# Kernel optimization log

Measured on AMD Instinct MI355X. Metric: run time of the kernel, lower is better.

The kernel has to match this reference:

```python
import jax, jax.numpy as jnp
import numpy as np

N_ENTITIES = 100000
N_USERS = 50000
CHANNEL = 64
N_RELATIONS = 16
N_FACTORS = 4
N_EDGES = 1600000
N_INTER = 1000000


def setup_inputs() -> dict:
    key = jax.random.key(0)
    ks = jax.random.split(key, 11)
    return {
        "entity_emb": jax.random.normal(ks[0], (N_ENTITIES, CHANNEL), dtype=jnp.float32),
        "user_emb": jax.random.normal(ks[1], (N_USERS, CHANNEL), dtype=jnp.float32),
        "latent_emb": jax.random.normal(ks[2], (N_FACTORS, CHANNEL), dtype=jnp.float32),
        "weight": jax.random.normal(ks[3], (N_RELATIONS, CHANNEL), dtype=jnp.float32),
        "disen_weight_att": jax.random.normal(ks[4], (N_FACTORS, N_RELATIONS), dtype=jnp.float32),
        "interact_vals": jax.random.uniform(ks[5], (N_INTER,), dtype=jnp.float32),
        "head": jax.random.randint(ks[6], (N_EDGES,), 0, N_ENTITIES),
        "tail": jax.random.randint(ks[7], (N_EDGES,), 0, N_ENTITIES),
        # edge_type is 1-indexed in the original (weight[edge_type - 1])
        "edge_type": jax.random.randint(ks[8], (N_EDGES,), 1, N_RELATIONS + 1),
        "interact_rows": jax.random.randint(ks[9], (N_INTER,), 0, N_USERS),
        "interact_cols": jax.random.randint(ks[10], (N_INTER,), 0, N_ENTITIES),
    }


def reference(entity_emb, user_emb, latent_emb, weight, disen_weight_att,
              interact_vals, head, tail, edge_type, interact_rows, interact_cols):
    # ---- KG aggregate (GATED_ATT branch, vectorized; chunk loop is math-identical) ----
    rel = weight[edge_type - 1]                                  # [E, C]
    att = jax.nn.sigmoid(jnp.sum(entity_emb[head] * rel, axis=1))[:, None]  # [E, 1]
    neigh = att * (entity_emb[tail] * rel)                       # [E, C]
    seg_sum = jax.ops.segment_sum(neigh, head, num_segments=N_ENTITIES)     # [N_e, C]
    cnt = jax.ops.segment_sum(jnp.ones_like(att[:, 0]), head, num_segments=N_ENTITIES)
    entity_agg = seg_sum / jnp.maximum(cnt, 1.0)[:, None]        # scatter_mean (0 if empty)

    # ---- user aggregate ----
    score = jax.nn.softmax(user_emb @ latent_emb.T, axis=1)[:, :, None]      # [U, F, 1]
    user_agg = jax.ops.segment_sum(interact_vals[:, None] * entity_emb[interact_cols],
                                   interact_rows, num_segments=N_USERS)      # sparse mm
    disen = jax.nn.softmax(disen_weight_att, axis=-1) @ weight               # [F, C]
    gate = jnp.sum(disen[None, :, :] * score, axis=1)                        # [U, C]
    user_agg = user_agg * gate + user_agg
    return entity_agg, user_agg
```

## Files before the change

### kernel.cpp

```cpp
#include <hip/hip_runtime.h>

#define N_ENTITIES 100000
#define N_USERS 50000
#define CHANNEL 64
#define N_RELATIONS 16
#define N_FACTORS 4
#define N_EDGES 1600000
#define N_INTER 1000000
#define TMASK ((1 << 17) - 1)

#define BSH 6
#define BSZ 64
#define NBE 1563
#define NBU 782
#define CAP_E 1536
#define CAP_U 1792
#define TILE_E 4096
#define TILE_U 4096
#define NTBE 391
#define NTBU 245
#define NCONV 6250
#define NHIST 256

typedef unsigned short u16;

__device__ __forceinline__ float wave_reduce_sum(float p) {
    #pragma unroll
    for (int off = 32; off > 0; off >>= 1) p += __shfl_xor(p, off);
    return p;
}

__device__ __forceinline__ int block_scan_incl(int v, int* wsum) {
    int lane = threadIdx.x & 63, wid = threadIdx.x >> 6;
    int x = v;
    #pragma unroll
    for (int off = 1; off < 64; off <<= 1) {
        int y = __shfl_up(x, off);
        if (lane >= off) x += y;
    }
    __syncthreads();
    if (lane == 63) wsum[wid] = x;
    __syncthreads();
    if (wid == 0) {
        int s = (lane < 16) ? wsum[lane] : 0;
        #pragma unroll
        for (int off = 1; off < 16; off <<= 1) {
            int y = __shfl_up(s, off);
            if (lane >= off) s += y;
        }
        if (lane < 16) wsum[lane] = s;
    }
    __syncthreads();
    return x + (wid ? wsum[wid - 1] : 0);
}

__device__ __forceinline__ u16 f32_to_bf16_rne(float x) {
    unsigned u = __float_as_uint(x);
    return (u16)((u + 0x7FFFu + ((u >> 16) & 1u)) >> 16);
}

template <bool BF16>
__device__ __forceinline__ float ldrow(const float* __restrict__ e32,
                                       const u16* __restrict__ e16,
                                       int row, int lane) {
    if (BF16) return __uint_as_float(((unsigned)e16[(size_t)row * CHANNEL + lane]) << 16);
    return e32[(size_t)row * CHANNEL + lane];
}

__device__ __forceinline__ void disen_body(const float* __restrict__ dwa,
                                           const float* __restrict__ weight,
                                           float* __restrict__ disen) {
    int f = threadIdx.x >> 6;
    int c = threadIdx.x & 63;
    float m = -INFINITY;
    #pragma unroll
    for (int r = 0; r < N_RELATIONS; ++r) m = fmaxf(m, dwa[f * N_RELATIONS + r]);
    float denom = 0.f, acc = 0.f;
    #pragma unroll
    for (int r = 0; r < N_RELATIONS; ++r) {
        float e = expf(dwa[f * N_RELATIONS + r] - m);
        denom += e;
        acc += e * weight[r * CHANNEL + c];
    }
    disen[f * CHANNEL + c] = acc / denom;
}

__global__ void disen_kernel(const float* __restrict__ dwa,
                             const float* __restrict__ weight,
                             float* __restrict__ disen) {
    disen_body(dwa, weight, disen);
}

__global__ __launch_bounds__(256) void prep_kernel(
    const float* __restrict__ src, u16* __restrict__ dst,
    const float* __restrict__ dwa, const float* __restrict__ weight,
    float* __restrict__ disen,
    const int* __restrict__ head, const int* __restrict__ irows,
    int* __restrict__ wp_e, int* __restrict__ wp_u) {
    __shared__ int lh[NBE + NBU];
    int bid = blockIdx.x;
    int tid = threadIdx.x;
    if (bid < NCONV) {
        int i = bid * 256 + tid;
        float4 v = ((const float4*)src)[i];
        ushort4 o;
        o.x = f32_to_bf16_rne(v.x);
        o.y = f32_to_bf16_rne(v.y);
        o.z = f32_to_bf16_rne(v.z);
        o.w = f32_to_bf16_rne(v.w);
        ((ushort4*)dst)[i] = o;
        return;
    }
    if (bid == NCONV) { disen_body(dwa, weight, disen); return; }
    for (int i = tid; i < NBE + NBU; i += 256) lh[i] = 0;
    __syncthreads();
    const int NTOT = N_EDGES + N_INTER;
    int hb = bid - NCONV - 1;
    for (int i = hb * 256 + tid; i < NTOT; i += NHIST * 256) {
        if (i < N_EDGES) atomicAdd(&lh[head[i] >> BSH], 1);
        else             atomicAdd(&lh[NBE + (irows[i - N_EDGES] >> BSH)], 1);
    }
    __syncthreads();
    for (int i = tid; i < NBE + NBU; i += 256) {
        int c = lh[i];
        if (c) {
            if (i < NBE) atomicAdd(&wp_e[i], c);
            else         atomicAdd(&wp_u[i - NBE], c);
        }
    }
}

__global__ __launch_bounds__(1024) void hist_kernel(
    const int* __restrict__ head, const int* __restrict__ irows,
    int* __restrict__ wp_e, int* __restrict__ wp_u) {
    __shared__ int lh[NBE + NBU];
    int tid = threadIdx.x;
    for (int i = tid; i < NBE + NBU; i += 1024) lh[i] = 0;
    __syncthreads();
    const int NTOT = N_EDGES + N_INTER;
    for (int i = blockIdx.x * 1024 + tid; i < NTOT; i += gridDim.x * 1024) {
        if (i < N_EDGES) atomicAdd(&lh[head[i] >> BSH], 1);
        else             atomicAdd(&lh[NBE + (irows[i - N_EDGES] >> BSH)], 1);
    }
    __syncthreads();
    for (int i = tid; i < NBE + NBU; i += 1024) {
        int c = lh[i];
        if (c) {
            if (i < NBE) atomicAdd(&wp_e[i], c);
            else         atomicAdd(&wp_u[i - NBE], c);
        }
    }
}

__global__ __launch_bounds__(1024) void scan_kernel(
    int* __restrict__ wp_e, int* __restrict__ coff_e,
    int* __restrict__ wp_u, int* __restrict__ coff_u) {
    __shared__ int wsum[16];
    int tid = threadIdx.x;
    int c0 = wp_e[tid];
    int incl0 = block_scan_incl(c0, wsum);
    int tot0 = wsum[15];
    int i1 = 1024 + tid;
    int c1 = (i1 < NBE) ? wp_e[i1] : 0;
    int incl1 = block_scan_incl(c1, wsum) + tot0;
    int cu = (tid < NBU) ? wp_u[tid] : 0;
    int inclu = block_scan_incl(cu, wsum);
    { int ex = incl0 - c0; coff_e[tid] = ex; wp_e[tid] = ex; }
    if (i1 < NBE) { int ex = incl1 - c1; coff_e[i1] = ex; wp_e[i1] = ex; }
    if (tid == 0) coff_e[NBE] = N_EDGES;
    if (tid < NBU) { int ex = inclu - cu; coff_u[tid] = ex; wp_u[tid] = ex; }
    if (tid == 0) coff_u[NBU] = N_INTER;
}

__global__ __launch_bounds__(1024) void scatter_kernel(
    const int* __restrict__ head, const int* __restrict__ tail,
    const int* __restrict__ etype,
    const int* __restrict__ irows, const int* __restrict__ icols,
    const float* __restrict__ vals,
    int* __restrict__ wp_e, int* __restrict__ pay_e,
    int* __restrict__ wp_u, int* __restrict__ payA_u, float* __restrict__ payB_u) {
    __shared__ __align__(16) char smem[58624];
    __shared__ int wsum[16];
    int tid = threadIdx.x;
    int bid = blockIdx.x;

    if (bid < NTBE) {
        int* s_hist  = (int*)smem;
        int* s_lofs  = s_hist + NBE;
        int* s_gbase = s_lofs + NBE;
        int* s_pay   = s_gbase + NBE;
        int* s_dest  = s_pay + TILE_E;
        int g0 = bid * TILE_E;
        int tilecnt = min(TILE_E, N_EDGES - g0);
        for (int i = tid; i < NBE; i += 1024) s_hist[i] = 0;
        int cb[4], pp[4], rk[4];
        __syncthreads();
        #pragma unroll
        for (int j = 0; j < 4; ++j) {
            int s = j * 1024 + tid;
            if (s < tilecnt) {
                int i = g0 + s;
                int h = head[i];
                cb[j] = h >> BSH;
                pp[j] = ((h & (BSZ - 1)) << 21) | ((etype[i] - 1) << 17) | tail[i];
            } else cb[j] = -1;
        }
        #pragma unroll
        for (int j = 0; j < 4; ++j)
            if (cb[j] >= 0) rk[j] = atomicAdd(&s_hist[cb[j]], 1);
        __syncthreads();
        int c0 = s_hist[tid];
        int incl0 = block_scan_incl(c0, wsum);
        int tot0 = wsum[15];
        int i1 = 1024 + tid;
        int c1 = (i1 < NBE) ? s_hist[i1] : 0;
        int incl1 = block_scan_incl(c1, wsum) + tot0;
        {
            int ex = incl0 - c0;
            s_lofs[tid] = ex;
            if (c0 > 0) s_gbase[tid] = atomicAdd(&wp_e[tid], c0) - ex;
        }
        if (i1 < NBE) {
            int ex = incl1 - c1;
            s_lofs[i1] = ex;
            if (c1 > 0) s_gbase[i1] = atomicAdd(&wp_e[i1], c1) - ex;
        }
        __syncthreads();
        #pragma unroll
        for (int j = 0; j < 4; ++j) {
            if (cb[j] >= 0) {
                int slot = s_lofs[cb[j]] + rk[j];
                s_pay[slot]  = pp[j];
                s_dest[slot] = s_gbase[cb[j]] + slot;
            }
        }
        __syncthreads();
        #pragma unroll
        for (int j = 0; j < 4; ++j) {
            int s = j * 1024 + tid;
            if (s < tilecnt) pay_e[s_dest[s]] = s_pay[s];
        }
    } else {
        int*   s_hist  = (int*)smem;
        int*   s_lofs  = s_hist + NBU;
        int*   s_gbase = s_lofs + NBU;
        int*   s_pay   = s_gbase + NBU;
        float* s_val   = (float*)(s_pay + TILE_U);
        int*   s_dest  = (int*)(s_val + TILE_U);
        int g0 = (bid - NTBE) * TILE_U;
        int tilecnt = min(TILE_U, N_INTER - g0);
        for (int i = tid; i < NBU; i += 1024) s_hist[i] = 0;
        int cb[4], pp[4], rk[4];
        float vv[4];
        __syncthreads();
        #pragma unroll
        for (int j = 0; j < 4; ++j) {
            int s = j * 1024 + tid;
            if (s < tilecnt) {
                int i = g0 + s;
                int u = irows[i];
                cb[j] = u >> BSH;
                pp[j] = ((u & (BSZ - 1)) << 17) | icols[i];
                vv[j] = vals[i];
            } else cb[j] = -1;
        }
        #pragma unroll
        for (int j = 0; j < 4; ++j)
            if (cb[j] >= 0) rk[j] = atomicAdd(&s_hist[cb[j]], 1);
        __syncthreads();
        int c0 = (tid < NBU) ? s_hist[tid] : 0;
        int incl0 = block_scan_incl(c0, wsum);
        if (tid < NBU) {
            int ex = incl0 - c0;
            s_lofs[tid] = ex;
            if (c0 > 0) s_gbase[tid] = atomicAdd(&wp_u[tid], c0) - ex;
        }
        __syncthreads();
        #pragma unroll
        for (int j = 0; j < 4; ++j) {
            if (cb[j] >= 0) {
                int slot = s_lofs[cb[j]] + rk[j];
                s_pay[slot]  = pp[j];
                s_val[slot]  = vv[j];
                s_dest[slot] = s_gbase[cb[j]] + slot;
            }
        }
        __syncthreads();
        #pragma unroll
        for (int j = 0; j < 4; ++j) {
            int s = j * 1024 + tid;
            if (s < tilecnt) {
                payA_u[s_dest[s]] = s_pay[s];
                payB_u[s_dest[s]] = s_val[s];
            }
        }
    }
}

template <bool BF16>
__global__ __launch_bounds__(256, 8) void gather_kernel(
    const float* __restrict__ entity_emb,
    const u16* __restrict__ emb16,
    const float* __restrict__ weight,
    const float* __restrict__ user_emb,
    const float* __restrict__ latent_emb,
    const float* __restrict__ disen,
    const int* __restrict__ coff_e,
    const int* __restrict__ pay_e,
    const int* __restrict__ coff_u,
    const int* __restrict__ payA_u,
    const float* __restrict__ payB_u,
    float* __restrict__ entity_agg,
    float* __restrict__ user_agg) {
    __shared__ __align__(16) char smem[16896];
    int tid = threadIdx.x;
    int wv = tid >> 6, lane = tid & 63;
    int bid = blockIdx.x;

    if (bid < NBE) {
        float* w65    = (float*)smem;
        float* s_attv = w65 + 1040;
        int*   s_pay  = (int*)(s_attv + 1024);
        int*   s_hist = s_pay + CAP_E;
        int*   s_scan = s_hist + 64;

        for (int i = tid; i < N_RELATIONS * CHANNEL; i += 256)
            w65[(i >> 6) * 65 + (i & 63)] = weight[i];
        if (tid < BSZ) s_hist[tid] = 0;
        int kbeg = coff_e[bid];
        int n = min(coff_e[bid + 1] - kbeg, CAP_E);
        __syncthreads();

        int myp[CAP_E / 256], myr[CAP_E / 256];
        #pragma unroll
        for (int j = 0; j < CAP_E / 256; ++j) {
            int s = j * 256 + tid;
            if (s < n) {
                int p = pay_e[kbeg + s];
                myp[j] = p;
                myr[j] = atomicAdd(&s_hist[p >> 21], 1);
            }
        }
        __syncthreads();
        if (wv == 0) {
            int x = s_hist[lane];
            #pragma unroll
            for (int off = 1; off < 64; off <<= 1) {
                int y = __shfl_up(x, off);
                if (lane >= off) x += y;
            }
            s_scan[lane] = x;
        }
        __syncthreads();
        #pragma unroll
        for (int j = 0; j < CAP_E / 256; ++j) {
            int s = j * 256 + tid;
            if (s < n) {
                int key = myp[j] >> 21;
                s_pay[s_scan[key] - s_hist[key] + myr[j]] = myp[j];
            }
        }

        int r = lane >> 2, q = lane & 3;
        for (int t = 0; t < 16; ++t) {
            int le = wv * 16 + t;
            int ge = bid * BSZ + le;
            if (ge >= N_ENTITIES) break;
            float eh = ldrow<BF16>(entity_emb, emb16, ge, lane);
            float p = 0.f;
            #pragma unroll
            for (int j = 0; j < 16; ++j)
                p += __shfl(eh, q * 16 + j) * w65[r * 65 + q * 16 + j];
            p += __shfl_xor(p, 1);
            p += __shfl_xor(p, 2);
            if (q == 0) s_attv[(le << 4) + r] = 1.f / (1.f + expf(-p));
        }
        __syncthreads();

        #define EBODY(K) { \
            int pp = s_pay[K]; \
            int et = (pp >> 17) & 15; \
            float v = ldrow<BF16>(entity_emb, emb16, pp & TMASK, lane); \
            acc += s_attv[(le << 4) + et] * v * w65[et * 65 + lane]; }
        for (int t = 0; t < 16; ++t) {
            int le = wv * 16 + t;
            int ge = bid * BSZ + le;
            if (ge >= N_ENTITIES) break;
            int cnt = s_hist[le];
            int ke = s_scan[le];
            int k = ke - cnt;
            float acc = 0.f;
            for (; k + 4 <= ke; k += 4) {
                EBODY(k); EBODY(k + 1); EBODY(k + 2); EBODY(k + 3);
            }
            for (; k < ke; ++k) EBODY(k);
            __builtin_nontemporal_store(acc / fmaxf((float)cnt, 1.0f),
                                        &entity_agg[(size_t)ge * CHANNEL + lane]);
        }
        #undef EBODY
    } else {
        int*   s_pay  = (int*)smem;
        float* s_val  = (float*)(s_pay + CAP_U);
        float* s_lat  = s_val + CAP_U;
        float* s_dis  = s_lat + 256;
        int*   s_hist = (int*)(s_dis + 256);
        int*   s_scan = s_hist + 64;

        if (tid < BSZ) s_hist[tid] = 0;
        if (tid < N_FACTORS * CHANNEL) {
            s_lat[tid] = latent_emb[tid];
            s_dis[tid] = disen[tid];
        }
        int b = bid - NBE;
        int kbeg = coff_u[b];
        int n = min(coff_u[b + 1] - kbeg, CAP_U);
        __syncthreads();

        int myp[CAP_U / 256], myr[CAP_U / 256];
        float myv[CAP_U / 256];
        #pragma unroll
        for (int j = 0; j < CAP_U / 256; ++j) {
            int s = j * 256 + tid;
            if (s < n) {
                int p = payA_u[kbeg + s];
                myp[j] = p;
                myv[j] = payB_u[kbeg + s];
                myr[j] = atomicAdd(&s_hist[p >> 17], 1);
            }
        }
        __syncthreads();
        if (wv == 0) {
            int x = s_hist[lane];
            #pragma unroll
            for (int off = 1; off < 64; off <<= 1) {
                int y = __shfl_up(x, off);
                if (lane >= off) x += y;
            }
            s_scan[lane] = x;
        }
        __syncthreads();
        #pragma unroll
        for (int j = 0; j < CAP_U / 256; ++j) {
            int s = j * 256 + tid;
            if (s < n) {
                int key = myp[j] >> 17;
                int slot = s_scan[key] - s_hist[key] + myr[j];
                s_pay[slot] = myp[j] & TMASK;
                s_val[slot] = myv[j];
            }
        }
        __syncthreads();

        #define UBODY(K) { \
            float v = ldrow<BF16>(entity_emb, emb16, s_pay[K], lane); \
            acc += s_val[K] * v; }
        for (int t = 0; t < 16; ++t) {
            int lu = wv * 16 + t;
            int gu = b * BSZ + lu;
            if (gu >= N_USERS) break;
            int cnt = s_hist[lu];
            int ke = s_scan[lu];
            int k = ke - cnt;
            float acc = 0.f;
            for (; k + 4 <= ke; k += 4) {
                UBODY(k); UBODY(k + 1); UBODY(k + 2); UBODY(k + 3);
            }
            for (; k < ke; ++k) UBODY(k);

            float ue = user_emb[(size_t)gu * CHANNEL + lane];
            float s[N_FACTORS];
            #pragma unroll
            for (int f = 0; f < N_FACTORS; ++f)
                s[f] = wave_reduce_sum(ue * s_lat[f * CHANNEL + lane]);
            float m = fmaxf(fmaxf(s[0], s[1]), fmaxf(s[2], s[3]));
            float d = 0.f;
            #pragma unroll
            for (int f = 0; f < N_FACTORS; ++f) { s[f] = expf(s[f] - m); d += s[f]; }
            float gate = 0.f;
            #pragma unroll
            for (int f = 0; f < N_FACTORS; ++f)
                gate += s_dis[f * CHANNEL + lane] * (s[f] / d);
            __builtin_nontemporal_store(acc * gate + acc,
                                        &user_agg[(size_t)gu * CHANNEL + lane]);
        }
        #undef UBODY
    }
}

extern "C" void kernel_launch(void* const* d_in, const int* in_sizes, int n_in,
                              void* d_out, int out_size, void* d_ws, size_t ws_size,
                              hipStream_t stream) {
    const float* entity_emb    = (const float*)d_in[0];
    const float* user_emb      = (const float*)d_in[1];
    const float* latent_emb    = (const float*)d_in[2];
    const float* weight        = (const float*)d_in[3];
    const float* dwa           = (const float*)d_in[4];
    const float* interact_vals = (const float*)d_in[5];
    const int*   head          = (const int*)d_in[6];
    const int*   tail          = (const int*)d_in[7];
    const int*   edge_type     = (const int*)d_in[8];
    const int*   irows         = (const int*)d_in[9];
    const int*   icols         = (const int*)d_in[10];

    float* entity_agg = (float*)d_out;
    float* user_agg   = (float*)d_out + (size_t)N_ENTITIES * CHANNEL;

    int*   wp_e   = (int*)d_ws;
    int*   wp_u   = wp_e + NBE;
    int*   coff_e = wp_u + NBU;
    int*   coff_u = coff_e + NBE + 1;
    int*   pay_e  = coff_u + NBU + 1;
    int*   payA_u = pay_e + N_EDGES;
    float* payB_u = (float*)(payA_u + N_INTER);
    float* disen  = payB_u + N_INTER;
    u16*   emb16  = (u16*)(disen + N_FACTORS * CHANNEL);

    size_t need_bf16 = (size_t)((char*)(emb16 + (size_t)N_ENTITIES * CHANNEL) - (char*)d_ws);
    bool use_bf16 = (ws_size >= need_bf16);
    if (!use_bf16) emb16 = (u16*)d_ws;

    hipMemsetAsync(wp_e, 0, (size_t)(NBE + NBU) * sizeof(int), stream);

    if (use_bf16) {
        prep_kernel<<<NCONV + 1 + NHIST, 256, 0, stream>>>(
            entity_emb, emb16, dwa, weight, disen, head, irows, wp_e, wp_u);
    } else {
        disen_kernel<<<1, 256, 0, stream>>>(dwa, weight, disen);
        hist_kernel<<<128, 1024, 0, stream>>>(head, irows, wp_e, wp_u);
    }

    scan_kernel<<<1, 1024, 0, stream>>>(wp_e, coff_e, wp_u, coff_u);

    scatter_kernel<<<NTBE + NTBU, 1024, 0, stream>>>(
        head, tail, edge_type, irows, icols, interact_vals,
        wp_e, pay_e, wp_u, payA_u, payB_u);

    if (use_bf16) {
        gather_kernel<true><<<NBE + NBU, 256, 0, stream>>>(
            entity_emb, emb16, weight, user_emb, latent_emb, disen,
            coff_e, pay_e, coff_u, payA_u, payB_u, entity_agg, user_agg);
    } else {
        gather_kernel<false><<<NBE + NBU, 256, 0, stream>>>(
            entity_emb, emb16, weight, user_emb, latent_emb, disen,
            coff_e, pay_e, coff_u, payA_u, payB_u, entity_agg, user_agg);
    }
}
```

Measured before the change: 199.3 us.

## Halve bucket size and use persistent gather blocks with atomic work queue

Shrinks the bucket granularity from 64 to 32 rows, which doubles the bucket counts and halves the scatter tiles. The scans are generalized into looped chunks to cover the larger bucket counts. The gather kernel becomes a persistent grid of 2048 blocks that pull bucket units from a global atomic counter and load weights, latent and disen tables into shared memory once per block. The inner gather loops are unrolled by 8 with all loads issued before the accumulates, to expose more memory-level parallelism. In exchange there are more scatter blocks, more per-unit synchronisation, and a dynamic-scheduling atomic per unit.

```diff
diff --git a/kernel.cpp b/kernel.cpp
--- a/kernel.cpp
+++ b/kernel.cpp
@@ -9,18 +9,19 @@
 #define N_INTER 1000000
 #define TMASK ((1 << 17) - 1)
 
-#define BSH 6
-#define BSZ 64
-#define NBE 1563
-#define NBU 782
-#define CAP_E 1536
-#define CAP_U 1792
-#define TILE_E 4096
-#define TILE_U 4096
-#define NTBE 391
-#define NTBU 245
+#define BSH 5
+#define BSZ 32
+#define NBE 3125
+#define NBU 1563
+#define CAP_E 768
+#define CAP_U 896
+#define TILE_E 2048
+#define TILE_U 2048
+#define NTBE 782
+#define NTBU 489
 #define NCONV 6250
 #define NHIST 256
+#define NWORK 2048
 
 typedef unsigned short u16;
 
@@ -157,18 +158,23 @@
     int* __restrict__ wp_u, int* __restrict__ coff_u) {
     __shared__ int wsum[16];
     int tid = threadIdx.x;
-    int c0 = wp_e[tid];
-    int incl0 = block_scan_incl(c0, wsum);
-    int tot0 = wsum[15];
-    int i1 = 1024 + tid;
-    int c1 = (i1 < NBE) ? wp_e[i1] : 0;
-    int incl1 = block_scan_incl(c1, wsum) + tot0;
-    int cu = (tid < NBU) ? wp_u[tid] : 0;
-    int inclu = block_scan_incl(cu, wsum);
-    { int ex = incl0 - c0; coff_e[tid] = ex; wp_e[tid] = ex; }
-    if (i1 < NBE) { int ex = incl1 - c1; coff_e[i1] = ex; wp_e[i1] = ex; }
+    int run = 0;
+    for (int c0 = 0; c0 < NBE; c0 += 1024) {
+        int i = c0 + tid;
+        int v = (i < NBE) ? wp_e[i] : 0;
+        int incl = block_scan_incl(v, wsum) + run;
+        run += wsum[15];
+        if (i < NBE) { int ex = incl - v; coff_e[i] = ex; wp_e[i] = ex; }
+    }
     if (tid == 0) coff_e[NBE] = N_EDGES;
-    if (tid < NBU) { int ex = inclu - cu; coff_u[tid] = ex; wp_u[tid] = ex; }
+    run = 0;
+    for (int c0 = 0; c0 < NBU; c0 += 1024) {
+        int i = c0 + tid;
+        int v = (i < NBU) ? wp_u[i] : 0;
+        int incl = block_scan_incl(v, wsum) + run;
+        run += wsum[15];
+        if (i < NBU) { int ex = incl - v; coff_u[i] = ex; wp_u[i] = ex; }
+    }
     if (tid == 0) coff_u[NBU] = N_INTER;
 }
 
@@ -179,7 +185,7 @@
     const float* __restrict__ vals,
     int* __restrict__ wp_e, int* __restrict__ pay_e,
     int* __restrict__ wp_u, int* __restrict__ payA_u, float* __restrict__ payB_u) {
-    __shared__ __align__(16) char smem[58624];
+    __shared__ __align__(16) char smem[53888];
     __shared__ int wsum[16];
     int tid = threadIdx.x;
     int bid = blockIdx.x;
@@ -193,10 +199,10 @@
         int g0 = bid * TILE_E;
         int tilecnt = min(TILE_E, N_EDGES - g0);
         for (int i = tid; i < NBE; i += 1024) s_hist[i] = 0;
-        int cb[4], pp[4], rk[4];
-        __syncthreads();
-        #pragma unroll
-        for (int j = 0; j < 4; ++j) {
+        int cb[2], pp[2], rk[2];
+        __syncthreads();
+        #pragma unroll
+        for (int j = 0; j < 2; ++j) {
             int s = j * 1024 + tid;
             if (s < tilecnt) {
                 int i = g0 + s;
@@ -206,28 +212,24 @@
             } else cb[j] = -1;
         }
         #pragma unroll
-        for (int j = 0; j < 4; ++j)
+        for (int j = 0; j < 2; ++j)
             if (cb[j] >= 0) rk[j] = atomicAdd(&s_hist[cb[j]], 1);
         __syncthreads();
-        int c0 = s_hist[tid];
-        int incl0 = block_scan_incl(c0, wsum);
-        int tot0 = wsum[15];
-        int i1 = 1024 + tid;
-        int c1 = (i1 < NBE) ? s_hist[i1] : 0;
-        int incl1 = block_scan_incl(c1, wsum) + tot0;
-        {
-            int ex = incl0 - c0;
-            s_lofs[tid] = ex;
-            if (c0 > 0) s_gbase[tid] = atomicAdd(&wp_e[tid], c0) - ex;
-        }
-        if (i1 < NBE) {
-            int ex = incl1 - c1;
-            s_lofs[i1] = ex;
-            if (c1 > 0) s_gbase[i1] = atomicAdd(&wp_e[i1], c1) - ex;
-        }
-        __syncthreads();
-        #pragma unroll
-        for (int j = 0; j < 4; ++j) {
+        int run = 0;
+        for (int c0 = 0; c0 < NBE; c0 += 1024) {
+            int i = c0 + tid;
+            int c = (i < NBE) ? s_hist[i] : 0;
+            int incl = block_scan_incl(c, wsum) + run;
+            run += wsum[15];
+            if (i < NBE) {
+                int ex = incl - c;
+                s_lofs[i] = ex;
+                if (c > 0) s_gbase[i] = atomicAdd(&wp_e[i], c) - ex;
+            }
+        }
+        __syncthreads();
+        #pragma unroll
+        for (int j = 0; j < 2; ++j) {
             if (cb[j] >= 0) {
                 int slot = s_lofs[cb[j]] + rk[j];
                 s_pay[slot]  = pp[j];
@@ -236,7 +238,7 @@
         }
         __syncthreads();
         #pragma unroll
-        for (int j = 0; j < 4; ++j) {
+        for (int j = 0; j < 2; ++j) {
             int s = j * 1024 + tid;
             if (s < tilecnt) pay_e[s_dest[s]] = s_pay[s];
         }
@@ -250,11 +252,11 @@
         int g0 = (bid - NTBE) * TILE_U;
         int tilecnt = min(TILE_U, N_INTER - g0);
         for (int i = tid; i < NBU; i += 1024) s_hist[i] = 0;
-        int cb[4], pp[4], rk[4];
-        float vv[4];
-        __syncthreads();
-        #pragma unroll
-        for (int j = 0; j < 4; ++j) {
+        int cb[2], pp[2], rk[2];
+        float vv[2];
+        __syncthreads();
+        #pragma unroll
+        for (int j = 0; j < 2; ++j) {
             int s = j * 1024 + tid;
             if (s < tilecnt) {
                 int i = g0 + s;
@@ -265,19 +267,24 @@
             } else cb[j] = -1;
         }
         #pragma unroll
-        for (int j = 0; j < 4; ++j)
+        for (int j = 0; j < 2; ++j)
             if (cb[j] >= 0) rk[j] = atomicAdd(&s_hist[cb[j]], 1);
         __syncthreads();
-        int c0 = (tid < NBU) ? s_hist[tid] : 0;
-        int incl0 = block_scan_incl(c0, wsum);
-        if (tid < NBU) {
-            int ex = incl0 - c0;
-            s_lofs[tid] = ex;
-            if (c0 > 0) s_gbase[tid] = atomicAdd(&wp_u[tid], c0) - ex;
-        }
-        __syncthreads();
-        #pragma unroll
-        for (int j = 0; j < 4; ++j) {
+        int run = 0;
+        for (int c0 = 0; c0 < NBU; c0 += 1024) {
+            int i = c0 + tid;
+            int c = (i < NBU) ? s_hist[i] : 0;
+            int incl = block_scan_incl(c, wsum) + run;
+            run += wsum[15];
+            if (i < NBU) {
+                int ex = incl - c;
+                s_lofs[i] = ex;
+                if (c > 0) s_gbase[i] = atomicAdd(&wp_u[i], c) - ex;
+            }
+        }
+        __syncthreads();
+        #pragma unroll
+        for (int j = 0; j < 2; ++j) {
             if (cb[j] >= 0) {
                 int slot = s_lofs[cb[j]] + rk[j];
                 s_pay[slot]  = pp[j];
@@ -287,7 +294,7 @@
         }
         __syncthreads();
         #pragma unroll
-        for (int j = 0; j < 4; ++j) {
+        for (int j = 0; j < 2; ++j) {
             int s = j * 1024 + tid;
             if (s < tilecnt) {
                 payA_u[s_dest[s]] = s_pay[s];
@@ -310,180 +317,200 @@
     const int* __restrict__ coff_u,
     const int* __restrict__ payA_u,
     const float* __restrict__ payB_u,
+    int* __restrict__ unit_ctr,
     float* __restrict__ entity_agg,
     float* __restrict__ user_agg) {
-    __shared__ __align__(16) char smem[16896];
+    __shared__ float w65[N_RELATIONS * 65];
+    __shared__ float s_lat[N_FACTORS * CHANNEL];
+    __shared__ float s_dis[N_FACTORS * CHANNEL];
+    __shared__ float s_attv[BSZ * N_RELATIONS];
+    __shared__ int   s_pay[CAP_U];
+    __shared__ float s_val[CAP_U];
+    __shared__ int   s_hist[BSZ], s_scan[BSZ];
+    __shared__ int   s_unit;
+
     int tid = threadIdx.x;
     int wv = tid >> 6, lane = tid & 63;
-    int bid = blockIdx.x;
-
-    if (bid < NBE) {
-        float* w65    = (float*)smem;
-        float* s_attv = w65 + 1040;
-        int*   s_pay  = (int*)(s_attv + 1024);
-        int*   s_hist = s_pay + CAP_E;
-        int*   s_scan = s_hist + 64;
-
-        for (int i = tid; i < N_RELATIONS * CHANNEL; i += 256)
-            w65[(i >> 6) * 65 + (i & 63)] = weight[i];
-        if (tid < BSZ) s_hist[tid] = 0;
-        int kbeg = coff_e[bid];
-        int n = min(coff_e[bid + 1] - kbeg, CAP_E);
-        __syncthreads();
-
-        int myp[CAP_E / 256], myr[CAP_E / 256];
-        #pragma unroll
-        for (int j = 0; j < CAP_E / 256; ++j) {
-            int s = j * 256 + tid;
-            if (s < n) {
-                int p = pay_e[kbeg + s];
-                myp[j] = p;
-                myr[j] = atomicAdd(&s_hist[p >> 21], 1);
-            }
-        }
-        __syncthreads();
-        if (wv == 0) {
-            int x = s_hist[lane];
+
+    for (int i = tid; i < N_RELATIONS * CHANNEL; i += 256)
+        w65[(i >> 6) * 65 + (i & 63)] = weight[i];
+    s_lat[tid] = latent_emb[tid];
+    s_dis[tid] = disen[tid];
+
+    for (;;) {
+        __syncthreads();
+        if (tid == 0) s_unit = atomicAdd(unit_ctr, 1);
+        __syncthreads();
+        int u = s_unit;
+        if (u >= NBE + NBU) break;
+
+        if (u < NBE) {
+            if (tid < BSZ) s_hist[tid] = 0;
+            int kbeg = coff_e[u];
+            int n = min(coff_e[u + 1] - kbeg, CAP_E);
+            __syncthreads();
+
+            int myp[CAP_E / 256], myr[CAP_E / 256];
             #pragma unroll
-            for (int off = 1; off < 64; off <<= 1) {
-                int y = __shfl_up(x, off);
-                if (lane >= off) x += y;
-            }
-            s_scan[lane] = x;
-        }
-        __syncthreads();
-        #pragma unroll
-        for (int j = 0; j < CAP_E / 256; ++j) {
-            int s = j * 256 + tid;
-            if (s < n) {
-                int key = myp[j] >> 21;
-                s_pay[s_scan[key] - s_hist[key] + myr[j]] = myp[j];
-            }
-        }
-
-        int r = lane >> 2, q = lane & 3;
-        for (int t = 0; t < 16; ++t) {
-            int le = wv * 16 + t;
-            int ge = bid * BSZ + le;
-            if (ge >= N_ENTITIES) break;
-            float eh = ldrow<BF16>(entity_emb, emb16, ge, lane);
-            float p = 0.f;
+            for (int j = 0; j < CAP_E / 256; ++j) {
+                int s = j * 256 + tid;
+                if (s < n) {
+                    int p = pay_e[kbeg + s];
+                    myp[j] = p;
+                    myr[j] = atomicAdd(&s_hist[p >> 21], 1);
+                }
+            }
+            __syncthreads();
+            if (tid < BSZ) {
+                int x = s_hist[tid];
+                #pragma unroll
+                for (int off = 1; off < BSZ; off <<= 1) {
+                    int y = __shfl_up(x, off);
+                    if (tid >= off) x += y;
+                }
+                s_scan[tid] = x;
+            }
+            __syncthreads();
             #pragma unroll
-            for (int j = 0; j < 16; ++j)
-                p += __shfl(eh, q * 16 + j) * w65[r * 65 + q * 16 + j];
-            p += __shfl_xor(p, 1);
-            p += __shfl_xor(p, 2);
-            if (q == 0) s_attv[(le << 4) + r] = 1.f / (1.f + expf(-p));
-        }
-        __syncthreads();
-
-        #define EBODY(K) { \
-            int pp = s_pay[K]; \
-            int et = (pp >> 17) & 15; \
-            float v = ldrow<BF16>(entity_emb, emb16, pp & TMASK, lane); \
-            acc += s_attv[(le << 4) + et] * v * w65[et * 65 + lane]; }
-        for (int t = 0; t < 16; ++t) {
-            int le = wv * 16 + t;
-            int ge = bid * BSZ + le;
-            if (ge >= N_ENTITIES) break;
-            int cnt = s_hist[le];
-            int ke = s_scan[le];
-            int k = ke - cnt;
-            float acc = 0.f;
-            for (; k + 4 <= ke; k += 4) {
-                EBODY(k); EBODY(k + 1); EBODY(k + 2); EBODY(k + 3);
-            }
-            for (; k < ke; ++k) EBODY(k);
-            __builtin_nontemporal_store(acc / fmaxf((float)cnt, 1.0f),
-                                        &entity_agg[(size_t)ge * CHANNEL + lane]);
-        }
-        #undef EBODY
-    } else {
-        int*   s_pay  = (int*)smem;
-        float* s_val  = (float*)(s_pay + CAP_U);
-        float* s_lat  = s_val + CAP_U;
-        float* s_dis  = s_lat + 256;
-        int*   s_hist = (int*)(s_dis + 256);
-        int*   s_scan = s_hist + 64;
-
-        if (tid < BSZ) s_hist[tid] = 0;
-        if (tid < N_FACTORS * CHANNEL) {
-            s_lat[tid] = latent_emb[tid];
-            s_dis[tid] = disen[tid];
-        }
-        int b = bid - NBE;
-        int kbeg = coff_u[b];
-        int n = min(coff_u[b + 1] - kbeg, CAP_U);
-        __syncthreads();
-
-        int myp[CAP_U / 256], myr[CAP_U / 256];
-        float myv[CAP_U / 256];
-        #pragma unroll
-        for (int j = 0; j < CAP_U / 256; ++j) {
-            int s = j * 256 + tid;
-            if (s < n) {
-                int p = payA_u[kbeg + s];
-                myp[j] = p;
-                myv[j] = payB_u[kbeg + s];
-                myr[j] = atomicAdd(&s_hist[p >> 17], 1);
-            }
-        }
-        __syncthreads();
-        if (wv == 0) {
-            int x = s_hist[lane];
+            for (int j = 0; j < CAP_E / 256; ++j) {
+                int s = j * 256 + tid;
+                if (s < n) {
+                    int key = myp[j] >> 21;
+                    s_pay[s_scan[key] - s_hist[key] + myr[j]] = myp[j];
+                }
+            }
+
+            int r = lane >> 2, q = lane & 3;
             #pragma unroll
-            for (int off = 1; off < 64; off <<= 1) {
-                int y = __shfl_up(x, off);
-                if (lane >= off) x += y;
-            }
-            s_scan[lane] = x;
-        }
-        __syncthreads();
-        #pragma unroll
-        for (int j = 0; j < CAP_U / 256; ++j) {
-            int s = j * 256 + tid;
-            if (s < n) {
-                int key = myp[j] >> 17;
-                int slot = s_scan[key] - s_hist[key] + myr[j];
-                s_pay[slot] = myp[j] & TMASK;
-                s_val[slot] = myv[j];
-            }
-        }
-        __syncthreads();
-
-        #define UBODY(K) { \
-            float v = ldrow<BF16>(entity_emb, emb16, s_pay[K], lane); \
-            acc += s_val[K] * v; }
-        for (int t = 0; t < 16; ++t) {
-            int lu = wv * 16 + t;
-            int gu = b * BSZ + lu;
-            if (gu >= N_USERS) break;
-            int cnt = s_hist[lu];
-            int ke = s_scan[lu];
-            int k = ke - cnt;
-            float acc = 0.f;
-            for (; k + 4 <= ke; k += 4) {
-                UBODY(k); UBODY(k + 1); UBODY(k + 2); UBODY(k + 3);
-            }
-            for (; k < ke; ++k) UBODY(k);
-
-            float ue = user_emb[(size_t)gu * CHANNEL + lane];
-            float s[N_FACTORS];
+            for (int t = 0; t < 8; ++t) {
+                int le = wv * 8 + t;
+                int ge = u * BSZ + le;
+                float eh = ldrow<BF16>(entity_emb, emb16, ge, lane);
+                float p = 0.f;
+                #pragma unroll
+                for (int j = 0; j < 16; ++j)
+                    p += __shfl(eh, q * 16 + j) * w65[r * 65 + q * 16 + j];
+                p += __shfl_xor(p, 1);
+                p += __shfl_xor(p, 2);
+                if (q == 0) s_attv[(le << 4) + r] = 1.f / (1.f + expf(-p));
+            }
+            __syncthreads();
+
+            #define ELD(i, K) int p##i = s_pay[K]; \
+                float v##i = ldrow<BF16>(entity_emb, emb16, p##i & TMASK, lane);
+            #define EACC(i) { int et = (p##i >> 17) & 15; \
+                acc += s_attv[(le << 4) + et] * v##i * w65[et * 65 + lane]; }
+            for (int t = 0; t < 8; ++t) {
+                int le = wv * 8 + t;
+                int ge = u * BSZ + le;
+                int cnt = s_hist[le];
+                int ke = s_scan[le];
+                int k = ke - cnt;
+                float acc = 0.f;
+                for (; k + 8 <= ke; k += 8) {
+                    ELD(0, k)     ELD(1, k + 1) ELD(2, k + 2) ELD(3, k + 3)
+                    ELD(4, k + 4) ELD(5, k + 5) ELD(6, k + 6) ELD(7, k + 7)
+                    EACC(0) EACC(1) EACC(2) EACC(3)
+                    EACC(4) EACC(5) EACC(6) EACC(7)
+                }
+                for (; k + 4 <= ke; k += 4) {
+                    ELD(0, k) ELD(1, k + 1) ELD(2, k + 2) ELD(3, k + 3)
+                    EACC(0) EACC(1) EACC(2) EACC(3)
+                }
+                for (; k < ke; ++k) {
+                    ELD(0, k)
+                    EACC(0)
+                }
+                __builtin_nontemporal_store(acc / fmaxf((float)cnt, 1.0f),
+                                            &entity_agg[(size_t)ge * CHANNEL + lane]);
+            }
+            #undef ELD
+            #undef EACC
+        } else {
+            int b = u - NBE;
+            if (tid < BSZ) s_hist[tid] = 0;
+            int kbeg = coff_u[b];
+            int n = min(coff_u[b + 1] - kbeg, CAP_U);
+            __syncthreads();
+
+            int myp[CAP_U / 256 + 1], myr[CAP_U / 256 + 1];
+            float myv[CAP_U / 256 + 1];
             #pragma unroll
-            for (int f = 0; f < N_FACTORS; ++f)
-                s[f] = wave_reduce_sum(ue * s_lat[f * CHANNEL + lane]);
-            float m = fmaxf(fmaxf(s[0], s[1]), fmaxf(s[2], s[3]));
-            float d = 0.f;
+            for (int j = 0; j < CAP_U / 256 + 1; ++j) {
+                int s = j * 256 + tid;
+                if (s < n) {
+                    int p = payA_u[kbeg + s];
+                    myp[j] = p;
+                    myv[j] = payB_u[kbeg + s];
+                    myr[j] = atomicAdd(&s_hist[p >> 17], 1);
+                }
+            }
+            __syncthreads();
+            if (tid < BSZ) {
+                int x = s_hist[tid];
+                #pragma unroll
+                for (int off = 1; off < BSZ; off <<= 1) {
+                    int y = __shfl_up(x, off);
+                    if (tid >= off) x += y;
+                }
+                s_scan[tid] = x;
+            }
+            __syncthreads();
             #pragma unroll
-            for (int f = 0; f < N_FACTORS; ++f) { s[f] = expf(s[f] - m); d += s[f]; }
-            float gate = 0.f;
-            #pragma unroll
-            for (int f = 0; f < N_FACTORS; ++f)
-                gate += s_dis[f * CHANNEL + lane] * (s[f] / d);
-            __builtin_nontemporal_store(acc * gate + acc,
-                                        &user_agg[(size_t)gu * CHANNEL + lane]);
-        }
-        #undef UBODY
+            for (int j = 0; j < CAP_U / 256 + 1; ++j) {
+                int s = j * 256 + tid;
+                if (s < n) {
+                    int key = myp[j] >> 17;
+                    int slot = s_scan[key] - s_hist[key] + myr[j];
+                    s_pay[slot] = myp[j] & TMASK;
+                    s_val[slot] = myv[j];
+                }
+            }
+            __syncthreads();
+
+            #define ULD(i, K) int c##i = s_pay[K]; float x##i = s_val[K]; \
+                float v##i = ldrow<BF16>(entity_emb, emb16, c##i, lane);
+            for (int t = 0; t < 8; ++t) {
+                int lu = wv * 8 + t;
+                int gu = b * BSZ + lu;
+                if (gu >= N_USERS) break;
+                int cnt = s_hist[lu];
+                int ke = s_scan[lu];
+                int k = ke - cnt;
+                float acc = 0.f;
+                for (; k + 8 <= ke; k += 8) {
+                    ULD(0, k)     ULD(1, k + 1) ULD(2, k + 2) ULD(3, k + 3)
+                    ULD(4, k + 4) ULD(5, k + 5) ULD(6, k + 6) ULD(7, k + 7)
+                    acc += x0 * v0 + x1 * v1 + x2 * v2 + x3 * v3;
+                    acc += x4 * v4 + x5 * v5 + x6 * v6 + x7 * v7;
+                }
+                for (; k + 4 <= ke; k += 4) {
+                    ULD(0, k) ULD(1, k + 1) ULD(2, k + 2) ULD(3, k + 3)
+                    acc += x0 * v0 + x1 * v1 + x2 * v2 + x3 * v3;
+                }
+                for (; k < ke; ++k) {
+                    ULD(0, k)
+                    acc += x0 * v0;
+                }
+
+                float ue = user_emb[(size_t)gu * CHANNEL + lane];
+                float s[N_FACTORS];
+                #pragma unroll
+                for (int f = 0; f < N_FACTORS; ++f)
+                    s[f] = wave_reduce_sum(ue * s_lat[f * CHANNEL + lane]);
+                float m = fmaxf(fmaxf(s[0], s[1]), fmaxf(s[2], s[3]));
+                float d = 0.f;
+                #pragma unroll
+                for (int f = 0; f < N_FACTORS; ++f) { s[f] = expf(s[f] - m); d += s[f]; }
+                float gate = 0.f;
+                #pragma unroll
+                for (int f = 0; f < N_FACTORS; ++f)
+                    gate += s_dis[f * CHANNEL + lane] * (s[f] / d);
+                __builtin_nontemporal_store(acc * gate + acc,
+                                            &user_agg[(size_t)gu * CHANNEL + lane]);
+            }
+            #undef ULD
+        }
     }
 }
 
@@ -507,7 +534,8 @@
 
     int*   wp_e   = (int*)d_ws;
     int*   wp_u   = wp_e + NBE;
-    int*   coff_e = wp_u + NBU;
+    int*   uctr   = wp_u + NBU;
+    int*   coff_e = uctr + 1;
     int*   coff_u = coff_e + NBE + 1;
     int*   pay_e  = coff_u + NBU + 1;
     int*   payA_u = pay_e + N_EDGES;
@@ -519,7 +547,7 @@
     bool use_bf16 = (ws_size >= need_bf16);
     if (!use_bf16) emb16 = (u16*)d_ws;
 
-    hipMemsetAsync(wp_e, 0, (size_t)(NBE + NBU) * sizeof(int), stream);
+    hipMemsetAsync(wp_e, 0, (size_t)(NBE + NBU + 1) * sizeof(int), stream);
 
     if (use_bf16) {
         prep_kernel<<<NCONV + 1 + NHIST, 256, 0, stream>>>(
@@ -536,12 +564,12 @@
         wp_e, pay_e, wp_u, payA_u, payB_u);
 
     if (use_bf16) {
-        gather_kernel<true><<<NBE + NBU, 256, 0, stream>>>(
+        gather_kernel<true><<<NWORK, 256, 0, stream>>>(
             entity_emb, emb16, weight, user_emb, latent_emb, disen,
-            coff_e, pay_e, coff_u, payA_u, payB_u, entity_agg, user_agg);
+            coff_e, pay_e, coff_u, payA_u, payB_u, uctr, entity_agg, user_agg);
     } else {
-        gather_kernel<false><<<NBE + NBU, 256, 0, stream>>>(
+        gather_kernel<false><<<NWORK, 256, 0, stream>>>(
             entity_emb, emb16, weight, user_emb, latent_emb, disen,
-            coff_e, pay_e, coff_u, payA_u, payB_u, entity_agg, user_agg);
-    }
-}
+            coff_e, pay_e, coff_u, payA_u, payB_u, uctr, entity_agg, user_agg);
+    }
+}
```

Result: slower. 236.4 us (+18.6%).
